# Kernel tuning notes

Hardware: AMD Instinct MI355X
Metric: run time of the kernel (lower is better)

## Reference

```python
import jax, jax.numpy as jnp
import numpy as np

WH, WW = 7, 7
N_HEADS = 6
INPUT_DIM = 192
HEAD_DIM = INPUT_DIM // N_HEADS
QK_SCALE = HEAD_DIM ** (-0.5)


def _relative_position_index(wh, ww):
    coords = np.stack(np.meshgrid(np.arange(wh), np.arange(ww), indexing='ij'))  # (2, wh, ww)
    cf = coords.reshape(2, -1)                       # (2, N)
    rel = cf[:, :, None] - cf[:, None, :]            # (2, N, N)
    rel = rel.transpose(1, 2, 0).copy()              # (N, N, 2)
    rel[:, :, 0] += wh - 1
    rel[:, :, 1] += ww - 1
    rel[:, :, 0] *= 2 * ww - 1
    return jnp.asarray(rel.sum(-1), dtype=jnp.int32)  # (N, N)

_REL_IDX = _relative_position_index(WH, WW)


def setup_inputs() -> dict:
    key = jax.random.key(0)
    ks = jax.random.split(key, 7)
    bW, nW = 4096, 64
    N = WH * WW
    s = 0.02
    return {
        "x": jax.random.normal(ks[0], (bW, WH, WW, INPUT_DIM), jnp.float32),
        "mask": jax.random.normal(ks[1], (nW, N, N), jnp.float32),
        "qkv_w": jax.random.normal(ks[2], (3 * INPUT_DIM, INPUT_DIM), jnp.float32) * s,
        "qkv_b": jax.random.normal(ks[3], (3 * INPUT_DIM,), jnp.float32) * s,
        "out_w": jax.random.normal(ks[4], (INPUT_DIM, INPUT_DIM), jnp.float32) * s,
        "out_b": jax.random.normal(ks[5], (INPUT_DIM,), jnp.float32) * s,
        "rpb_table": jax.random.normal(ks[6], ((2 * WH - 1) * (2 * WW - 1), N_HEADS), jnp.float32) * s,
    }


def reference(x, mask, qkv_w, qkv_b, out_w, out_b, rpb_table):
    b, Wh, Ww, C = x.shape
    N = Wh * Ww
    H, D = N_HEADS, HEAD_DIM
    # 1x1 conv == pointwise linear over channels-last input
    qkv = jnp.einsum('bxyc,oc->bxyo', x, qkv_w) + qkv_b          # (b, Wh, Ww, 3C)
    qkv = qkv.reshape(b, N, 3, H, D)                             # chunk order q,k,v; (h d) channel layout
    q, k, v = qkv[:, :, 0], qkv[:, :, 1], qkv[:, :, 2]           # (b, N, H, D)
    q = q * QK_SCALE
    sim = jnp.einsum('bihd,bjhd->bhij', q, k)                    # (b, H, N, N)
    # relative position bias gather
    rpb = rpb_table[_REL_IDX]                                    # (N, N, H)
    sim = sim + rpb.transpose(2, 0, 1)[None]                     # + (1, H, N, N)
    # shift mask add over windows
    nW = mask.shape[0]
    sim = sim.reshape(b // nW, nW, H, N, N) + mask[None, :, None]
    attn = jax.nn.softmax(sim, axis=-1).reshape(b, H, N, N)
    out = jnp.einsum('bhij,bjhd->bihd', attn, v)                 # (b, N, H, D)
    out = out.reshape(b, N, H * D)                               # (h d) channel order
    out = jnp.einsum('bnc,oc->bno', out, out_w) + out_b
    return out.reshape(b, Wh, Ww, C)
```

## Files before the change

kernel.cpp:

```cpp
#include <hip/hip_runtime.h>
#include <hip/hip_bf16.h>

typedef __bf16 bf16;
typedef __bf16 bf16x8 __attribute__((ext_vector_type(8)));
typedef float f32x4 __attribute__((ext_vector_type(4)));
typedef float floatv4 __attribute__((ext_vector_type(4)));

#define QK_SCALE 0.17677669529663687f

__device__ __forceinline__ bf16* qk_ptr(bf16* base, int row, int col) {
    return base + row * 32 + ((((col >> 3) ^ ((row >> 1) & 3)) << 3)) + (col & 7);
}
__device__ __forceinline__ bf16* vt_ptr(bf16* base, int row, int col) {
    return base + row * 64 + ((((col >> 3) ^ (row & 7)) << 3)) + (col & 7);
}
__device__ __forceinline__ bf16* ao_ptr(bf16* base, int row, int col) {
    return base + row * 192 + ((((col >> 3) ^ (row & 7)) << 3)) + (col & 7);
}

__global__ void wmsa_prep(const float* __restrict__ qkv_w,
                          const float* __restrict__ out_w,
                          const float* __restrict__ rpb_table,
                          const float* __restrict__ mask,
                          bf16* __restrict__ qkv_wb,
                          bf16* __restrict__ out_wb,
                          float* __restrict__ rpbx,
                          float* __restrict__ combo,
                          int build_combo) {
    int t = blockIdx.x * 256 + threadIdx.x;
    if (t < 110592) qkv_wb[t] = (bf16)qkv_w[t];
    if (t < 36864)  out_wb[t] = (bf16)out_w[t];
    if (t < 14406) {
        int h = t / 2401, ij = t % 2401, i = ij / 49, j = ij % 49;
        int ri = (i / 7 - j / 7 + 6) * 13 + (i % 7 - j % 7 + 6);
        rpbx[t] = rpb_table[ri * 6 + h];
    }
    if (build_combo && t < 64 * 6 * 64 * 64) {
        int j = t & 63, i = (t >> 6) & 63, r = t >> 12;
        int h = r % 6, w = r / 6;
        float v = -1e30f;
        if (i < 49 && j < 49) {
            int ri = (i / 7 - j / 7 + 6) * 13 + (i % 7 - j % 7 + 6);
            v = rpb_table[ri * 6 + h] + mask[w * 2401 + i * 49 + j];
        }
        combo[t] = v;
    }
}

template <bool USE_COMBO>
__global__ __launch_bounds__(768, 3) void wmsa_fused(
    const float* __restrict__ x, const float* __restrict__ mask,
    const float* __restrict__ qkv_b, const float* __restrict__ out_b,
    const bf16* __restrict__ qkv_wb, const bf16* __restrict__ out_wb,
    const float* __restrict__ rpbx, const float* __restrict__ combo,
    float* __restrict__ out)
{
    __shared__ __align__(16) bf16 s_x[12288];
    __shared__ __align__(16) bf16 s_qp[6][2048];
    __shared__ __align__(16) bf16 s_kao[12288];
    __shared__ __align__(16) bf16 s_vt[6][2048];

    const int b    = blockIdx.x;
    const int tid  = threadIdx.x;
    const int wv   = tid >> 6;
    const int lane = tid & 63;
    const int lo   = lane & 15;
    const int hi   = lane >> 4;

    const float* xw    = x + (size_t)b * 9408;
    const int    obase = wv * 48;
    const int    sec   = wv >> 2;

    {
        const int c0 = tid;
        const int r0s = c0 / 24, cc0 = c0 % 24;
        const float* p0 = xw + r0s * 192 + cc0 * 8;
        floatv4 f0 = *(const floatv4*)p0;
        floatv4 f1 = *(const floatv4*)(p0 + 4);
        bf16x8 v;
        v[0]=(bf16)f0[0]; v[1]=(bf16)f0[1]; v[2]=(bf16)f0[2]; v[3]=(bf16)f0[3];
        v[4]=(bf16)f1[0]; v[5]=(bf16)f1[1]; v[6]=(bf16)f1[2]; v[7]=(bf16)f1[3];
        *(bf16x8*)&s_x[(r0s * 24 + (cc0 ^ (r0s & 7))) * 8] = v;

        const int c1 = tid + 768;
        const int r1s = c1 / 24, cc1 = c1 % 24;
        bf16x8 w = {};
        if (r1s < 49) {
            const float* p1 = xw + r1s * 192 + cc1 * 8;
            floatv4 g0 = *(const floatv4*)p1;
            floatv4 g1 = *(const floatv4*)(p1 + 4);
            w[0]=(bf16)g0[0]; w[1]=(bf16)g0[1]; w[2]=(bf16)g0[2]; w[3]=(bf16)g0[3];
            w[4]=(bf16)g1[0]; w[5]=(bf16)g1[1]; w[6]=(bf16)g1[2]; w[7]=(bf16)g1[3];
        }
        *(bf16x8*)&s_x[(r1s * 24 + (cc1 ^ (r1s & 7))) * 8] = w;
    }
    __syncthreads();

#pragma unroll 1
    for (int mib = 0; mib < 2; ++mib) {
        f32x4 acc[2][3];
#pragma unroll
        for (int mi = 0; mi < 2; ++mi)
#pragma unroll
            for (int nj = 0; nj < 3; ++nj) acc[mi][nj] = (f32x4){0.f, 0.f, 0.f, 0.f};

        const int r0 = mib * 32 + lo;
        const int r1 = r0 + 16;

        auto loadB = [&](bf16x8* dst, int kk) {
#pragma unroll
            for (int nj = 0; nj < 3; ++nj)
                dst[nj] = *(const bf16x8*)(qkv_wb + (obase + nj * 16 + lo) * 192 + kk * 32 + hi * 8);
        };

        bf16x8 b0_[3], b1_[3], b2_[3];
        loadB(b0_, 0);
        loadB(b1_, 1);
#pragma unroll
        for (int kk = 0; kk < 6; ++kk) {
            if (kk < 4) loadB(b2_, kk + 2);
            bf16x8 a0 = *(const bf16x8*)ao_ptr(s_x, r0, kk * 32 + hi * 8);
            bf16x8 a1 = *(const bf16x8*)ao_ptr(s_x, r1, kk * 32 + hi * 8);
            acc[0][0] = __builtin_amdgcn_mfma_f32_16x16x32_bf16(a0, b0_[0], acc[0][0], 0, 0, 0);
            acc[1][0] = __builtin_amdgcn_mfma_f32_16x16x32_bf16(a1, b0_[0], acc[1][0], 0, 0, 0);
            acc[0][1] = __builtin_amdgcn_mfma_f32_16x16x32_bf16(a0, b0_[1], acc[0][1], 0, 0, 0);
            acc[1][1] = __builtin_amdgcn_mfma_f32_16x16x32_bf16(a1, b0_[1], acc[1][1], 0, 0, 0);
            acc[0][2] = __builtin_amdgcn_mfma_f32_16x16x32_bf16(a0, b0_[2], acc[0][2], 0, 0, 0);
            acc[1][2] = __builtin_amdgcn_mfma_f32_16x16x32_bf16(a1, b0_[2], acc[1][2], 0, 0, 0);
            b0_[0] = b1_[0]; b0_[1] = b1_[1]; b0_[2] = b1_[2];
            b1_[0] = b2_[0]; b1_[1] = b2_[1]; b1_[2] = b2_[2];
        }

#pragma unroll
        for (int nj = 0; nj < 3; ++nj) {
            const int o    = obase + nj * 16 + lo;
            const float bs = qkv_b[o];
            const int oc   = o - sec * 192;
            const int hh   = oc >> 5;
            const int dd   = oc & 31;
#pragma unroll
            for (int mi = 0; mi < 2; ++mi)
#pragma unroll
                for (int r = 0; r < 4; ++r) {
                    const int n = mib * 32 + mi * 16 + hi * 4 + r;
                    const float v = acc[mi][nj][r] + bs;
                    if (sec == 0)      *qk_ptr(&s_qp[hh][0], n, dd)      = (bf16)(v * QK_SCALE);
                    else if (sec == 1) *qk_ptr(s_kao + hh * 2048, n, dd) = (bf16)v;
                    else               *vt_ptr(&s_vt[hh][0], dd, n)      = (bf16)v;
                }
        }
    }
    __syncthreads();

    {
        const int h    = wv >> 1;
        const int p    = wv & 1;
        const int rowb = p * 32;
        bf16* qb    = &s_qp[h][0];
        bf16* kbase = s_kao + h * 2048;

        f32x4 cv[2][4];
        if (USE_COMBO) {
            const float* cb = combo + (((size_t)(b & 63) * 6 + h) << 12);
#pragma unroll
            for (int mi = 0; mi < 2; ++mi)
#pragma unroll
                for (int nt = 0; nt < 4; ++nt)
#pragma unroll
                    for (int r = 0; r < 4; ++r)
                        cv[mi][nt][r] = cb[(rowb + mi * 16 + hi * 4 + r) * 64 + nt * 16 + lo];
        }

        bf16x8 qa0 = *(const bf16x8*)qk_ptr(qb, rowb + lo, hi * 8);
        bf16x8 qa1 = *(const bf16x8*)qk_ptr(qb, rowb + 16 + lo, hi * 8);
        bf16x8 kb0 = *(const bf16x8*)qk_ptr(kbase,  0 + lo, hi * 8);
        bf16x8 kb1 = *(const bf16x8*)qk_ptr(kbase, 16 + lo, hi * 8);
        bf16x8 kb2 = *(const bf16x8*)qk_ptr(kbase, 32 + lo, hi * 8);
        bf16x8 kb3 = *(const bf16x8*)qk_ptr(kbase, 48 + lo, hi * 8);

        __syncthreads();

        f32x4 s[2][4];
#pragma unroll
        for (int mi = 0; mi < 2; ++mi)
#pragma unroll
            for (int nt = 0; nt < 4; ++nt) s[mi][nt] = (f32x4){0.f, 0.f, 0.f, 0.f};
        s[0][0] = __builtin_amdgcn_mfma_f32_16x16x32_bf16(qa0, kb0, s[0][0], 0, 0, 0);
        s[0][1] = __builtin_amdgcn_mfma_f32_16x16x32_bf16(qa0, kb1, s[0][1], 0, 0, 0);
        s[0][2] = __builtin_amdgcn_mfma_f32_16x16x32_bf16(qa0, kb2, s[0][2], 0, 0, 0);
        s[0][3] = __builtin_amdgcn_mfma_f32_16x16x32_bf16(qa0, kb3, s[0][3], 0, 0, 0);
        s[1][0] = __builtin_amdgcn_mfma_f32_16x16x32_bf16(qa1, kb0, s[1][0], 0, 0, 0);
        s[1][1] = __builtin_amdgcn_mfma_f32_16x16x32_bf16(qa1, kb1, s[1][1], 0, 0, 0);
        s[1][2] = __builtin_amdgcn_mfma_f32_16x16x32_bf16(qa1, kb2, s[1][2], 0, 0, 0);
        s[1][3] = __builtin_amdgcn_mfma_f32_16x16x32_bf16(qa1, kb3, s[1][3], 0, 0, 0);

        if (USE_COMBO) {
#pragma unroll
            for (int mi = 0; mi < 2; ++mi)
#pragma unroll
                for (int nt = 0; nt < 4; ++nt) s[mi][nt] += cv[mi][nt];
        } else {
            const float* mk = mask + (size_t)(b & 63) * 2401;
            const float* rb = rpbx + h * 2401;
#pragma unroll
            for (int nt = 0; nt < 4; ++nt) {
                const int j = nt * 16 + lo;
#pragma unroll
                for (int mi = 0; mi < 2; ++mi)
#pragma unroll
                    for (int r = 0; r < 4; ++r) {
                        const int i = rowb + mi * 16 + hi * 4 + r;
                        float sv = s[mi][nt][r];
                        if (j >= 49 || i >= 49) sv = -1e30f;
                        else sv += rb[i * 49 + j] + mk[i * 49 + j];
                        s[mi][nt][r] = sv;
                    }
            }
        }

#pragma unroll
        for (int mi = 0; mi < 2; ++mi)
#pragma unroll
            for (int r = 0; r < 4; ++r) {
                float m = fmaxf(fmaxf(s[mi][0][r], s[mi][1][r]),
                                fmaxf(s[mi][2][r], s[mi][3][r]));
                m = fmaxf(m, __shfl_xor(m, 1));
                m = fmaxf(m, __shfl_xor(m, 2));
                m = fmaxf(m, __shfl_xor(m, 4));
                m = fmaxf(m, __shfl_xor(m, 8));
                float sum = 0.f;
#pragma unroll
                for (int nt = 0; nt < 4; ++nt) {
                    float pv = __expf(s[mi][nt][r] - m);
                    s[mi][nt][r] = pv;
                    sum += pv;
                }
                sum += __shfl_xor(sum, 1);
                sum += __shfl_xor(sum, 2);
                sum += __shfl_xor(sum, 4);
                sum += __shfl_xor(sum, 8);
                const float inv = 1.0f / sum;
#pragma unroll
                for (int nt = 0; nt < 4; ++nt) s[mi][nt][r] *= inv;
            }

        f32x4 o00 = (f32x4){0.f,0.f,0.f,0.f}, o01 = (f32x4){0.f,0.f,0.f,0.f};
        f32x4 o10 = (f32x4){0.f,0.f,0.f,0.f}, o11 = (f32x4){0.f,0.f,0.f,0.f};
#pragma unroll
        for (int kk = 0; kk < 2; ++kk) {
#pragma unroll
            for (int mi = 0; mi < 2; ++mi)
#pragma unroll
                for (int c = 0; c < 2; ++c) {
                    const int nt = kk * 2 + c;
#pragma unroll
                    for (int r = 0; r < 4; ++r)
                        *qk_ptr(qb, rowb + mi * 16 + hi * 4 + r, c * 16 + lo) =
                            (bf16)s[mi][nt][r];
                }
            bf16x8 pa0 = *(const bf16x8*)qk_ptr(qb, rowb + lo, hi * 8);
            bf16x8 pa1 = *(const bf16x8*)qk_ptr(qb, rowb + 16 + lo, hi * 8);
            bf16x8 vb0 = *(const bf16x8*)vt_ptr(&s_vt[h][0],  0 + lo, kk * 32 + hi * 8);
            bf16x8 vb1 = *(const bf16x8*)vt_ptr(&s_vt[h][0], 16 + lo, kk * 32 + hi * 8);
            o00 = __builtin_amdgcn_mfma_f32_16x16x32_bf16(pa0, vb0, o00, 0, 0, 0);
            o10 = __builtin_amdgcn_mfma_f32_16x16x32_bf16(pa1, vb0, o10, 0, 0, 0);
            o01 = __builtin_amdgcn_mfma_f32_16x16x32_bf16(pa0, vb1, o01, 0, 0, 0);
            o11 = __builtin_amdgcn_mfma_f32_16x16x32_bf16(pa1, vb1, o11, 0, 0, 0);
        }

#pragma unroll
        for (int r = 0; r < 4; ++r) {
            const int n0 = rowb + hi * 4 + r;
            const int n1 = n0 + 16;
            *ao_ptr(s_kao, n0, h * 32 +  0 + lo) = (bf16)o00[r];
            *ao_ptr(s_kao, n0, h * 32 + 16 + lo) = (bf16)o01[r];
            *ao_ptr(s_kao, n1, h * 32 +  0 + lo) = (bf16)o10[r];
            *ao_ptr(s_kao, n1, h * 32 + 16 + lo) = (bf16)o11[r];
        }
    }
    __syncthreads();

    {
        const int o2 = wv * 16 + lo;
        f32x4 facc[4];
#pragma unroll
        for (int mi = 0; mi < 4; ++mi) facc[mi] = (f32x4){0.f, 0.f, 0.f, 0.f};

        bf16x8 fbc = *(const bf16x8*)(out_wb + o2 * 192 + hi * 8);
#pragma unroll
        for (int kk = 0; kk < 6; ++kk) {
            bf16x8 fbn;
            if (kk < 5) fbn = *(const bf16x8*)(out_wb + o2 * 192 + (kk + 1) * 32 + hi * 8);
            bf16x8 fa[4];
#pragma unroll
            for (int mi = 0; mi < 4; ++mi)
                fa[mi] = *(const bf16x8*)ao_ptr(s_kao, mi * 16 + lo, kk * 32 + hi * 8);
#pragma unroll
            for (int mi = 0; mi < 4; ++mi)
                facc[mi] = __builtin_amdgcn_mfma_f32_16x16x32_bf16(fa[mi], fbc, facc[mi], 0, 0, 0);
            fbc = fbn;
        }

        const float ob = out_b[o2];
        float* ow = out + (size_t)b * 9408;
#pragma unroll
        for (int mi = 0; mi < 4; ++mi)
#pragma unroll
            for (int r = 0; r < 4; ++r) {
                const int n = mi * 16 + hi * 4 + r;
                if (n < 49) ow[n * 192 + o2] = facc[mi][r] + ob;
            }
    }
}

extern "C" void kernel_launch(void* const* d_in, const int* in_sizes, int n_in,
                              void* d_out, int out_size, void* d_ws, size_t ws_size,
                              hipStream_t stream) {
    const float* x      = (const float*)d_in[0];
    const float* mask   = (const float*)d_in[1];
    const float* qkv_w  = (const float*)d_in[2];
    const float* qkv_b  = (const float*)d_in[3];
    const float* out_w  = (const float*)d_in[4];
    const float* out_b  = (const float*)d_in[5];
    const float* rpb    = (const float*)d_in[6];
    float* out          = (float*)d_out;

    char* ws = (char*)d_ws;
    bf16*  qkv_wb = (bf16*)ws;
    bf16*  out_wb = (bf16*)(ws + 221184);
    float* rpbx   = (float*)(ws + 294912);
    float* combo  = (float*)(ws + 352768);
    const bool use_combo = ws_size >= (size_t)(352768 + 6291456);

    hipLaunchKernelGGL(wmsa_prep, dim3(6144), dim3(256), 0, stream,
                       qkv_w, out_w, rpb, mask, qkv_wb, out_wb, rpbx, combo,
                       use_combo ? 1 : 0);
    if (use_combo)
        hipLaunchKernelGGL(HIP_KERNEL_NAME(wmsa_fused<true>), dim3(4096), dim3(768), 0, stream,
                           x, mask, qkv_b, out_b, qkv_wb, out_wb, rpbx, combo, out);
    else
        hipLaunchKernelGGL(HIP_KERNEL_NAME(wmsa_fused<false>), dim3(4096), dim3(768), 0, stream,
                           x, mask, qkv_b, out_b, qkv_wb, out_wb, rpbx, combo, out);
}
```

Baseline: 309.0 us.

## Make fused WMSA kernel persistent over 16 windows with double-buffered x prefetch

```diff
diff --git a/kernel.cpp b/kernel.cpp
--- a/kernel.cpp
+++ b/kernel.cpp
@@ -6,7 +6,8 @@
 typedef float f32x4 __attribute__((ext_vector_type(4)));
 typedef float floatv4 __attribute__((ext_vector_type(4)));
 
-#define QK_SCALE 0.17677669529663687f
+#define LOG2E 1.4426950408889634f
+#define QK_SCALE2 (0.17677669529663687f * 1.4426950408889634f)
 
 __device__ __forceinline__ bf16* qk_ptr(bf16* base, int row, int col) {
     return base + row * 32 + ((((col >> 3) ^ ((row >> 1) & 3)) << 3)) + (col & 7);
@@ -14,7 +15,7 @@
 __device__ __forceinline__ bf16* vt_ptr(bf16* base, int row, int col) {
     return base + row * 64 + ((((col >> 3) ^ (row & 7)) << 3)) + (col & 7);
 }
-__device__ __forceinline__ bf16* ao_ptr(bf16* base, int row, int col) {
+__device__ __forceinline__ bf16* t192_ptr(bf16* base, int row, int col) {
     return base + row * 192 + ((((col >> 3) ^ (row & 7)) << 3)) + (col & 7);
 }
 
@@ -41,11 +42,13 @@
         float v = -1e30f;
         if (i < 49 && j < 49) {
             int ri = (i / 7 - j / 7 + 6) * 13 + (i % 7 - j % 7 + 6);
-            v = rpb_table[ri * 6 + h] + mask[w * 2401 + i * 49 + j];
+            v = (rpb_table[ri * 6 + h] + mask[w * 2401 + i * 49 + j]) * LOG2E;
         }
         combo[t] = v;
     }
 }
+
+#define WIN_PER_BLK 16
 
 template <bool USE_COMBO>
 __global__ __launch_bounds__(768, 3) void wmsa_fused(
@@ -55,261 +58,295 @@
     const float* __restrict__ rpbx, const float* __restrict__ combo,
     float* __restrict__ out)
 {
-    __shared__ __align__(16) bf16 s_x[12288];
+    __shared__ __align__(16) bf16 s_x[2][12288];
     __shared__ __align__(16) bf16 s_qp[6][2048];
     __shared__ __align__(16) bf16 s_kao[12288];
     __shared__ __align__(16) bf16 s_vt[6][2048];
 
-    const int b    = blockIdx.x;
     const int tid  = threadIdx.x;
     const int wv   = tid >> 6;
     const int lane = tid & 63;
     const int lo   = lane & 15;
     const int hi   = lane >> 4;
 
-    const float* xw    = x + (size_t)b * 9408;
-    const int    obase = wv * 48;
-    const int    sec   = wv >> 2;
+    const int obase = wv * 48;
+    const int sec   = wv >> 2;
+    const int ah    = wv >> 1;
+    const int arow  = (wv & 1) * 32;
+
+    const int pr0 = tid / 24,         pcc0 = tid % 24;
+    const int pr1 = (tid + 768) / 24, pcc1 = (tid + 768) % 24;
+
+    const int bbase = blockIdx.x * WIN_PER_BLK;
 
     {
-        const int c0 = tid;
-        const int r0s = c0 / 24, cc0 = c0 % 24;
-        const float* p0 = xw + r0s * 192 + cc0 * 8;
+        const float* xw = x + (size_t)bbase * 9408;
+        const float* p0 = xw + pr0 * 192 + pcc0 * 8;
         floatv4 f0 = *(const floatv4*)p0;
         floatv4 f1 = *(const floatv4*)(p0 + 4);
         bf16x8 v;
         v[0]=(bf16)f0[0]; v[1]=(bf16)f0[1]; v[2]=(bf16)f0[2]; v[3]=(bf16)f0[3];
         v[4]=(bf16)f1[0]; v[5]=(bf16)f1[1]; v[6]=(bf16)f1[2]; v[7]=(bf16)f1[3];
-        *(bf16x8*)&s_x[(r0s * 24 + (cc0 ^ (r0s & 7))) * 8] = v;
-
-        const int c1 = tid + 768;
-        const int r1s = c1 / 24, cc1 = c1 % 24;
+        *(bf16x8*)&s_x[0][(pr0 * 24 + (pcc0 ^ (pr0 & 7))) * 8] = v;
+
         bf16x8 w = {};
-        if (r1s < 49) {
-            const float* p1 = xw + r1s * 192 + cc1 * 8;
+        if (pr1 < 49) {
+            const float* p1 = xw + pr1 * 192 + pcc1 * 8;
             floatv4 g0 = *(const floatv4*)p1;
             floatv4 g1 = *(const floatv4*)(p1 + 4);
             w[0]=(bf16)g0[0]; w[1]=(bf16)g0[1]; w[2]=(bf16)g0[2]; w[3]=(bf16)g0[3];
             w[4]=(bf16)g1[0]; w[5]=(bf16)g1[1]; w[6]=(bf16)g1[2]; w[7]=(bf16)g1[3];
         }
-        *(bf16x8*)&s_x[(r1s * 24 + (cc1 ^ (r1s & 7))) * 8] = w;
+        *(bf16x8*)&s_x[0][(pr1 * 24 + (pcc1 ^ (pr1 & 7))) * 8] = w;
     }
-    __syncthreads();
 
 #pragma unroll 1
-    for (int mib = 0; mib < 2; ++mib) {
-        f32x4 acc[2][3];
-#pragma unroll
-        for (int mi = 0; mi < 2; ++mi)
-#pragma unroll
-            for (int nj = 0; nj < 3; ++nj) acc[mi][nj] = (f32x4){0.f, 0.f, 0.f, 0.f};
-
-        const int r0 = mib * 32 + lo;
-        const int r1 = r0 + 16;
-
-        auto loadB = [&](bf16x8* dst, int kk) {
-#pragma unroll
-            for (int nj = 0; nj < 3; ++nj)
-                dst[nj] = *(const bf16x8*)(qkv_wb + (obase + nj * 16 + lo) * 192 + kk * 32 + hi * 8);
-        };
-
-        bf16x8 b0_[3], b1_[3], b2_[3];
-        loadB(b0_, 0);
-        loadB(b1_, 1);
-#pragma unroll
-        for (int kk = 0; kk < 6; ++kk) {
-            if (kk < 4) loadB(b2_, kk + 2);
-            bf16x8 a0 = *(const bf16x8*)ao_ptr(s_x, r0, kk * 32 + hi * 8);
-            bf16x8 a1 = *(const bf16x8*)ao_ptr(s_x, r1, kk * 32 + hi * 8);
-            acc[0][0] = __builtin_amdgcn_mfma_f32_16x16x32_bf16(a0, b0_[0], acc[0][0], 0, 0, 0);
-            acc[1][0] = __builtin_amdgcn_mfma_f32_16x16x32_bf16(a1, b0_[0], acc[1][0], 0, 0, 0);
-            acc[0][1] = __builtin_amdgcn_mfma_f32_16x16x32_bf16(a0, b0_[1], acc[0][1], 0, 0, 0);
-            acc[1][1] = __builtin_amdgcn_mfma_f32_16x16x32_bf16(a1, b0_[1], acc[1][1], 0, 0, 0);
-            acc[0][2] = __builtin_amdgcn_mfma_f32_16x16x32_bf16(a0, b0_[2], acc[0][2], 0, 0, 0);
-            acc[1][2] = __builtin_amdgcn_mfma_f32_16x16x32_bf16(a1, b0_[2], acc[1][2], 0, 0, 0);
-            b0_[0] = b1_[0]; b0_[1] = b1_[1]; b0_[2] = b1_[2];
-            b1_[0] = b2_[0]; b1_[1] = b2_[1]; b1_[2] = b2_[2];
-        }
-
-#pragma unroll
-        for (int nj = 0; nj < 3; ++nj) {
-            const int o    = obase + nj * 16 + lo;
-            const float bs = qkv_b[o];
-            const int oc   = o - sec * 192;
-            const int hh   = oc >> 5;
-            const int dd   = oc & 31;
+    for (int it = 0; it < WIN_PER_BLK; ++it) {
+        const int b = bbase + it;
+        bf16* sx = &s_x[it & 1][0];
+
+        __syncthreads();
+
+#pragma unroll 1
+        for (int mib = 0; mib < 2; ++mib) {
+            f32x4 acc[2][3];
 #pragma unroll
             for (int mi = 0; mi < 2; ++mi)
 #pragma unroll
+                for (int nj = 0; nj < 3; ++nj) acc[mi][nj] = (f32x4){0.f, 0.f, 0.f, 0.f};
+
+            const int r0 = mib * 32 + lo;
+            const int r1 = r0 + 16;
+
+            auto loadB = [&](bf16x8* dst, int kk) {
+#pragma unroll
+                for (int nj = 0; nj < 3; ++nj)
+                    dst[nj] = *(const bf16x8*)(qkv_wb + (obase + nj * 16 + lo) * 192 + kk * 32 + hi * 8);
+            };
+
+            bf16x8 b0_[3], b1_[3], b2_[3];
+            loadB(b0_, 0);
+            loadB(b1_, 1);
+#pragma unroll
+            for (int kk = 0; kk < 6; ++kk) {
+                if (kk < 4) loadB(b2_, kk + 2);
+                bf16x8 a0 = *(const bf16x8*)t192_ptr(sx, r0, kk * 32 + hi * 8);
+                bf16x8 a1 = *(const bf16x8*)t192_ptr(sx, r1, kk * 32 + hi * 8);
+                acc[0][0] = __builtin_amdgcn_mfma_f32_16x16x32_bf16(a0, b0_[0], acc[0][0], 0, 0, 0);
+                acc[1][0] = __builtin_amdgcn_mfma_f32_16x16x32_bf16(a1, b0_[0], acc[1][0], 0, 0, 0);
+                acc[0][1] = __builtin_amdgcn_mfma_f32_16x16x32_bf16(a0, b0_[1], acc[0][1], 0, 0, 0);
+                acc[1][1] = __builtin_amdgcn_mfma_f32_16x16x32_bf16(a1, b0_[1], acc[1][1], 0, 0, 0);
+                acc[0][2] = __builtin_amdgcn_mfma_f32_16x16x32_bf16(a0, b0_[2], acc[0][2], 0, 0, 0);
+                acc[1][2] = __builtin_amdgcn_mfma_f32_16x16x32_bf16(a1, b0_[2], acc[1][2], 0, 0, 0);
+                b0_[0] = b1_[0]; b0_[1] = b1_[1]; b0_[2] = b1_[2];
+                b1_[0] = b2_[0]; b1_[1] = b2_[1]; b1_[2] = b2_[2];
+            }
+
+#pragma unroll
+            for (int nj = 0; nj < 3; ++nj) {
+                const int o    = obase + nj * 16 + lo;
+                const float bs = qkv_b[o];
+                const int oc   = o - sec * 192;
+                const int hh   = oc >> 5;
+                const int dd   = oc & 31;
+#pragma unroll
+                for (int mi = 0; mi < 2; ++mi)
+#pragma unroll
+                    for (int r = 0; r < 4; ++r) {
+                        const int n = mib * 32 + mi * 16 + hi * 4 + r;
+                        const float v = acc[mi][nj][r] + bs;
+                        if (sec == 0)      *qk_ptr(&s_qp[hh][0], n, dd)      = (bf16)(v * QK_SCALE2);
+                        else if (sec == 1) *qk_ptr(s_kao + hh * 2048, n, dd) = (bf16)v;
+                        else               *vt_ptr(&s_vt[hh][0], dd, n)      = (bf16)v;
+                    }
+            }
+        }
+        __syncthreads();
+
+        {
+            bf16* qb    = &s_qp[ah][0];
+            bf16* kbase = s_kao + ah * 2048;
+
+            f32x4 cv[2][4];
+            if (USE_COMBO) {
+                const float* cb = combo + (((size_t)(b & 63) * 6 + ah) << 12);
+#pragma unroll
+                for (int mi = 0; mi < 2; ++mi)
+#pragma unroll
+                    for (int nt = 0; nt < 4; ++nt)
+#pragma unroll
+                        for (int r = 0; r < 4; ++r)
+                            cv[mi][nt][r] = cb[(arow + mi * 16 + hi * 4 + r) * 64 + nt * 16 + lo];
+            }
+
+            bf16x8 qa0 = *(const bf16x8*)qk_ptr(qb, arow + lo, hi * 8);
+            bf16x8 qa1 = *(const bf16x8*)qk_ptr(qb, arow + 16 + lo, hi * 8);
+            bf16x8 kb0 = *(const bf16x8*)qk_ptr(kbase,  0 + lo, hi * 8);
+            bf16x8 kb1 = *(const bf16x8*)qk_ptr(kbase, 16 + lo, hi * 8);
+            bf16x8 kb2 = *(const bf16x8*)qk_ptr(kbase, 32 + lo, hi * 8);
+            bf16x8 kb3 = *(const bf16x8*)qk_ptr(kbase, 48 + lo, hi * 8);
+
+            __syncthreads();
+
+            f32x4 s[2][4];
+#pragma unroll
+            for (int mi = 0; mi < 2; ++mi)
+#pragma unroll
+                for (int nt = 0; nt < 4; ++nt) s[mi][nt] = (f32x4){0.f, 0.f, 0.f, 0.f};
+            s[0][0] = __builtin_amdgcn_mfma_f32_16x16x32_bf16(qa0, kb0, s[0][0], 0, 0, 0);
+            s[0][1] = __builtin_amdgcn_mfma_f32_16x16x32_bf16(qa0, kb1, s[0][1], 0, 0, 0);
+            s[0][2] = __builtin_amdgcn_mfma_f32_16x16x32_bf16(qa0, kb2, s[0][2], 0, 0, 0);
+            s[0][3] = __builtin_amdgcn_mfma_f32_16x16x32_bf16(qa0, kb3, s[0][3], 0, 0, 0);
+            s[1][0] = __builtin_amdgcn_mfma_f32_16x16x32_bf16(qa1, kb0, s[1][0], 0, 0, 0);
+            s[1][1] = __builtin_amdgcn_mfma_f32_16x16x32_bf16(qa1, kb1, s[1][1], 0, 0, 0);
+            s[1][2] = __builtin_amdgcn_mfma_f32_16x16x32_bf16(qa1, kb2, s[1][2], 0, 0, 0);
+            s[1][3] = __builtin_amdgcn_mfma_f32_16x16x32_bf16(qa1, kb3, s[1][3], 0, 0, 0);
+
+            if (USE_COMBO) {
+#pragma unroll
+                for (int mi = 0; mi < 2; ++mi)
+#pragma unroll
+                    for (int nt = 0; nt < 4; ++nt) s[mi][nt] += cv[mi][nt];
+            } else {
+                const float* mk = mask + (size_t)(b & 63) * 2401;
+                const float* rb = rpbx + ah * 2401;
+#pragma unroll
+                for (int nt = 0; nt < 4; ++nt) {
+                    const int j = nt * 16 + lo;
+#pragma unroll
+                    for (int mi = 0; mi < 2; ++mi)
+#pragma unroll
+                        for (int r = 0; r < 4; ++r) {
+                            const int i = arow + mi * 16 + hi * 4 + r;
+                            float sv = s[mi][nt][r];
+                            if (j >= 49 || i >= 49) sv = -1e30f;
+                            else sv += (rb[i * 49 + j] + mk[i * 49 + j]) * LOG2E;
+                            s[mi][nt][r] = sv;
+                        }
+                }
+            }
+
+#pragma unroll
+            for (int mi = 0; mi < 2; ++mi)
+#pragma unroll
                 for (int r = 0; r < 4; ++r) {
-                    const int n = mib * 32 + mi * 16 + hi * 4 + r;
-                    const float v = acc[mi][nj][r] + bs;
-                    if (sec == 0)      *qk_ptr(&s_qp[hh][0], n, dd)      = (bf16)(v * QK_SCALE);
-                    else if (sec == 1) *qk_ptr(s_kao + hh * 2048, n, dd) = (bf16)v;
-                    else               *vt_ptr(&s_vt[hh][0], dd, n)      = (bf16)v;
+                    float m = fmaxf(fmaxf(s[mi][0][r], s[mi][1][r]),
+                                    fmaxf(s[mi][2][r], s[mi][3][r]));
+                    m = fmaxf(m, __shfl_xor(m, 1));
+                    m = fmaxf(m, __shfl_xor(m, 2));
+                    m = fmaxf(m, __shfl_xor(m, 4));
+                    m = fmaxf(m, __shfl_xor(m, 8));
+                    float sum = 0.f;
+#pragma unroll
+                    for (int nt = 0; nt < 4; ++nt) {
+                        float pv = exp2f(s[mi][nt][r] - m);
+                        s[mi][nt][r] = pv;
+                        sum += pv;
+                    }
+                    sum += __shfl_xor(sum, 1);
+                    sum += __shfl_xor(sum, 2);
+                    sum += __shfl_xor(sum, 4);
+                    sum += __shfl_xor(sum, 8);
+                    const float inv = 1.0f / sum;
+#pragma unroll
+                    for (int nt = 0; nt < 4; ++nt) s[mi][nt][r] *= inv;
                 }
-        }
-    }
-    __syncthreads();
-
-    {
-        const int h    = wv >> 1;
-        const int p    = wv & 1;
-        const int rowb = p * 32;
-        bf16* qb    = &s_qp[h][0];
-        bf16* kbase = s_kao + h * 2048;
-
-        f32x4 cv[2][4];
-        if (USE_COMBO) {
-            const float* cb = combo + (((size_t)(b & 63) * 6 + h) << 12);
-#pragma unroll
-            for (int mi = 0; mi < 2; ++mi)
-#pragma unroll
-                for (int nt = 0; nt < 4; ++nt)
-#pragma unroll
-                    for (int r = 0; r < 4; ++r)
-                        cv[mi][nt][r] = cb[(rowb + mi * 16 + hi * 4 + r) * 64 + nt * 16 + lo];
-        }
-
-        bf16x8 qa0 = *(const bf16x8*)qk_ptr(qb, rowb + lo, hi * 8);
-        bf16x8 qa1 = *(const bf16x8*)qk_ptr(qb, rowb + 16 + lo, hi * 8);
-        bf16x8 kb0 = *(const bf16x8*)qk_ptr(kbase,  0 + lo, hi * 8);
-        bf16x8 kb1 = *(const bf16x8*)qk_ptr(kbase, 16 + lo, hi * 8);
-        bf16x8 kb2 = *(const bf16x8*)qk_ptr(kbase, 32 + lo, hi * 8);
-        bf16x8 kb3 = *(const bf16x8*)qk_ptr(kbase, 48 + lo, hi * 8);
-
+
+            f32x4 o00 = (f32x4){0.f,0.f,0.f,0.f}, o01 = (f32x4){0.f,0.f,0.f,0.f};
+            f32x4 o10 = (f32x4){0.f,0.f,0.f,0.f}, o11 = (f32x4){0.f,0.f,0.f,0.f};
+#pragma unroll
+            for (int kk = 0; kk < 2; ++kk) {
+#pragma unroll
+                for (int mi = 0; mi < 2; ++mi)
+#pragma unroll
+                    for (int c = 0; c < 2; ++c) {
+                        const int nt = kk * 2 + c;
+#pragma unroll
+                        for (int r = 0; r < 4; ++r)
+                            *qk_ptr(qb, arow + mi * 16 + hi * 4 + r, c * 16 + lo) =
+                                (bf16)s[mi][nt][r];
+                    }
+                bf16x8 pa0 = *(const bf16x8*)qk_ptr(qb, arow + lo, hi * 8);
+                bf16x8 pa1 = *(const bf16x8*)qk_ptr(qb, arow + 16 + lo, hi * 8);
+                bf16x8 vb0 = *(const bf16x8*)vt_ptr(&s_vt[ah][0],  0 + lo, kk * 32 + hi * 8);
+                bf16x8 vb1 = *(const bf16x8*)vt_ptr(&s_vt[ah][0], 16 + lo, kk * 32 + hi * 8);
+                o00 = __builtin_amdgcn_mfma_f32_16x16x32_bf16(pa0, vb0, o00, 0, 0, 0);
+                o10 = __builtin_amdgcn_mfma_f32_16x16x32_bf16(pa1, vb0, o10, 0, 0, 0);
+                o01 = __builtin_amdgcn_mfma_f32_16x16x32_bf16(pa0, vb1, o01, 0, 0, 0);
+                o11 = __builtin_amdgcn_mfma_f32_16x16x32_bf16(pa1, vb1, o11, 0, 0, 0);
+            }
+
+#pragma unroll
+            for (int r = 0; r < 4; ++r) {
+                const int n0 = arow + hi * 4 + r;
+                const int n1 = n0 + 16;
+                *t192_ptr(s_kao, n0, ah * 32 +  0 + lo) = (bf16)o00[r];
+                *t192_ptr(s_kao, n0, ah * 32 + 16 + lo) = (bf16)o01[r];
+                *t192_ptr(s_kao, n1, ah * 32 +  0 + lo) = (bf16)o10[r];
+                *t192_ptr(s_kao, n1, ah * 32 + 16 + lo) = (bf16)o11[r];
+            }
+        }
         __syncthreads();
 
-        f32x4 s[2][4];
-#pragma unroll
-        for (int mi = 0; mi < 2; ++mi)
-#pragma unroll
-            for (int nt = 0; nt < 4; ++nt) s[mi][nt] = (f32x4){0.f, 0.f, 0.f, 0.f};
-        s[0][0] = __builtin_amdgcn_mfma_f32_16x16x32_bf16(qa0, kb0, s[0][0], 0, 0, 0);
-        s[0][1] = __builtin_amdgcn_mfma_f32_16x16x32_bf16(qa0, kb1, s[0][1], 0, 0, 0);
-        s[0][2] = __builtin_amdgcn_mfma_f32_16x16x32_bf16(qa0, kb2, s[0][2], 0, 0, 0);
-        s[0][3] = __builtin_amdgcn_mfma_f32_16x16x32_bf16(qa0, kb3, s[0][3], 0, 0, 0);
-        s[1][0] = __builtin_amdgcn_mfma_f32_16x16x32_bf16(qa1, kb0, s[1][0], 0, 0, 0);
-        s[1][1] = __builtin_amdgcn_mfma_f32_16x16x32_bf16(qa1, kb1, s[1][1], 0, 0, 0);
-        s[1][2] = __builtin_amdgcn_mfma_f32_16x16x32_bf16(qa1, kb2, s[1][2], 0, 0, 0);
-        s[1][3] = __builtin_amdgcn_mfma_f32_16x16x32_bf16(qa1, kb3, s[1][3], 0, 0, 0);
-
-        if (USE_COMBO) {
-#pragma unroll
-            for (int mi = 0; mi < 2; ++mi)
-#pragma unroll
-                for (int nt = 0; nt < 4; ++nt) s[mi][nt] += cv[mi][nt];
-        } else {
-            const float* mk = mask + (size_t)(b & 63) * 2401;
-            const float* rb = rpbx + h * 2401;
-#pragma unroll
-            for (int nt = 0; nt < 4; ++nt) {
-                const int j = nt * 16 + lo;
-#pragma unroll
-                for (int mi = 0; mi < 2; ++mi)
-#pragma unroll
-                    for (int r = 0; r < 4; ++r) {
-                        const int i = rowb + mi * 16 + hi * 4 + r;
-                        float sv = s[mi][nt][r];
-                        if (j >= 49 || i >= 49) sv = -1e30f;
-                        else sv += rb[i * 49 + j] + mk[i * 49 + j];
-                        s[mi][nt][r] = sv;
-                    }
-            }
-        }
-
-#pragma unroll
-        for (int mi = 0; mi < 2; ++mi)
-#pragma unroll
-            for (int r = 0; r < 4; ++r) {
-                float m = fmaxf(fmaxf(s[mi][0][r], s[mi][1][r]),
-                                fmaxf(s[mi][2][r], s[mi][3][r]));
-                m = fmaxf(m, __shfl_xor(m, 1));
-                m = fmaxf(m, __shfl_xor(m, 2));
-                m = fmaxf(m, __shfl_xor(m, 4));
-                m = fmaxf(m, __shfl_xor(m, 8));
-                float sum = 0.f;
-#pragma unroll
-                for (int nt = 0; nt < 4; ++nt) {
-                    float pv = __expf(s[mi][nt][r] - m);
-                    s[mi][nt][r] = pv;
-                    sum += pv;
+        floatv4 pf00, pf01, pf10, pf11;
+        const bool do_pf = (it + 1 < WIN_PER_BLK);
+        if (do_pf) {
+            const float* xn = x + (size_t)(b + 1) * 9408;
+            const float* p0 = xn + pr0 * 192 + pcc0 * 8;
+            pf00 = *(const floatv4*)p0;
+            pf01 = *(const floatv4*)(p0 + 4);
+            pf10 = (floatv4){0.f,0.f,0.f,0.f};
+            pf11 = (floatv4){0.f,0.f,0.f,0.f};
+            if (pr1 < 49) {
+                const float* p1 = xn + pr1 * 192 + pcc1 * 8;
+                pf10 = *(const floatv4*)p1;
+                pf11 = *(const floatv4*)(p1 + 4);
+            }
+        }
+
+        {
+            const int o2 = wv * 16 + lo;
+            f32x4 facc[4];
+#pragma unroll
+            for (int mi = 0; mi < 4; ++mi) facc[mi] = (f32x4){0.f, 0.f, 0.f, 0.f};
+
+            bf16x8 fbc = *(const bf16x8*)(out_wb + o2 * 192 + hi * 8);
+#pragma unroll
+            for (int kk = 0; kk < 6; ++kk) {
+                bf16x8 fbn;
+                if (kk < 5) fbn = *(const bf16x8*)(out_wb + o2 * 192 + (kk + 1) * 32 + hi * 8);
+                bf16x8 fa[4];
+#pragma unroll
+                for (int mi = 0; mi < 4; ++mi)
+                    fa[mi] = *(const bf16x8*)t192_ptr(s_kao, mi * 16 + lo, kk * 32 + hi * 8);
+#pragma unroll
+                for (int mi = 0; mi < 4; ++mi)
+                    facc[mi] = __builtin_amdgcn_mfma_f32_16x16x32_bf16(fa[mi], fbc, facc[mi], 0, 0, 0);
+                fbc = fbn;
+            }
+
+            const float ob = out_b[o2];
+            float* ow = out + (size_t)b * 9408;
+#pragma unroll
+            for (int mi = 0; mi < 4; ++mi)
+#pragma unroll
+                for (int r = 0; r < 4; ++r) {
+                    const int n = mi * 16 + hi * 4 + r;
+                    if (n < 49) ow[n * 192 + o2] = facc[mi][r] + ob;
                 }
-                sum += __shfl_xor(sum, 1);
-                sum += __shfl_xor(sum, 2);
-                sum += __shfl_xor(sum, 4);
-                sum += __shfl_xor(sum, 8);
-                const float inv = 1.0f / sum;
-#pragma unroll
-                for (int nt = 0; nt < 4; ++nt) s[mi][nt][r] *= inv;
-            }
-
-        f32x4 o00 = (f32x4){0.f,0.f,0.f,0.f}, o01 = (f32x4){0.f,0.f,0.f,0.f};
-        f32x4 o10 = (f32x4){0.f,0.f,0.f,0.f}, o11 = (f32x4){0.f,0.f,0.f,0.f};
-#pragma unroll
-        for (int kk = 0; kk < 2; ++kk) {
-#pragma unroll
-            for (int mi = 0; mi < 2; ++mi)
-#pragma unroll
-                for (int c = 0; c < 2; ++c) {
-                    const int nt = kk * 2 + c;
-#pragma unroll
-                    for (int r = 0; r < 4; ++r)
-                        *qk_ptr(qb, rowb + mi * 16 + hi * 4 + r, c * 16 + lo) =
-                            (bf16)s[mi][nt][r];
-                }
-            bf16x8 pa0 = *(const bf16x8*)qk_ptr(qb, rowb + lo, hi * 8);
-            bf16x8 pa1 = *(const bf16x8*)qk_ptr(qb, rowb + 16 + lo, hi * 8);
-            bf16x8 vb0 = *(const bf16x8*)vt_ptr(&s_vt[h][0],  0 + lo, kk * 32 + hi * 8);
-            bf16x8 vb1 = *(const bf16x8*)vt_ptr(&s_vt[h][0], 16 + lo, kk * 32 + hi * 8);
-            o00 = __builtin_amdgcn_mfma_f32_16x16x32_bf16(pa0, vb0, o00, 0, 0, 0);
-            o10 = __builtin_amdgcn_mfma_f32_16x16x32_bf16(pa1, vb0, o10, 0, 0, 0);
-            o01 = __builtin_amdgcn_mfma_f32_16x16x32_bf16(pa0, vb1, o01, 0, 0, 0);
-            o11 = __builtin_amdgcn_mfma_f32_16x16x32_bf16(pa1, vb1, o11, 0, 0, 0);
-        }
-
-#pragma unroll
-        for (int r = 0; r < 4; ++r) {
-            const int n0 = rowb + hi * 4 + r;
-            const int n1 = n0 + 16;
-            *ao_ptr(s_kao, n0, h * 32 +  0 + lo) = (bf16)o00[r];
-            *ao_ptr(s_kao, n0, h * 32 + 16 + lo) = (bf16)o01[r];
-            *ao_ptr(s_kao, n1, h * 32 +  0 + lo) = (bf16)o10[r];
-            *ao_ptr(s_kao, n1, h * 32 + 16 + lo) = (bf16)o11[r];
-        }
-    }
-    __syncthreads();
-
-    {
-        const int o2 = wv * 16 + lo;
-        f32x4 facc[4];
-#pragma unroll
-        for (int mi = 0; mi < 4; ++mi) facc[mi] = (f32x4){0.f, 0.f, 0.f, 0.f};
-
-        bf16x8 fbc = *(const bf16x8*)(out_wb + o2 * 192 + hi * 8);
-#pragma unroll
-        for (int kk = 0; kk < 6; ++kk) {
-            bf16x8 fbn;
-            if (kk < 5) fbn = *(const bf16x8*)(out_wb + o2 * 192 + (kk + 1) * 32 + hi * 8);
-            bf16x8 fa[4];
-#pragma unroll
-            for (int mi = 0; mi < 4; ++mi)
-                fa[mi] = *(const bf16x8*)ao_ptr(s_kao, mi * 16 + lo, kk * 32 + hi * 8);
-#pragma unroll
-            for (int mi = 0; mi < 4; ++mi)
-                facc[mi] = __builtin_amdgcn_mfma_f32_16x16x32_bf16(fa[mi], fbc, facc[mi], 0, 0, 0);
-            fbc = fbn;
-        }
-
-        const float ob = out_b[o2];
-        float* ow = out + (size_t)b * 9408;
-#pragma unroll
-        for (int mi = 0; mi < 4; ++mi)
-#pragma unroll
-            for (int r = 0; r < 4; ++r) {
-                const int n = mi * 16 + hi * 4 + r;
-                if (n < 49) ow[n * 192 + o2] = facc[mi][r] + ob;
-            }
+        }
+
+        if (do_pf) {
+            bf16* xb = &s_x[(it + 1) & 1][0];
+            bf16x8 v;
+            v[0]=(bf16)pf00[0]; v[1]=(bf16)pf00[1]; v[2]=(bf16)pf00[2]; v[3]=(bf16)pf00[3];
+            v[4]=(bf16)pf01[0]; v[5]=(bf16)pf01[1]; v[6]=(bf16)pf01[2]; v[7]=(bf16)pf01[3];
+            *(bf16x8*)&xb[(pr0 * 24 + (pcc0 ^ (pr0 & 7))) * 8] = v;
+            bf16x8 w;
+            w[0]=(bf16)pf10[0]; w[1]=(bf16)pf10[1]; w[2]=(bf16)pf10[2]; w[3]=(bf16)pf10[3];
+            w[4]=(bf16)pf11[0]; w[5]=(bf16)pf11[1]; w[6]=(bf16)pf11[2]; w[7]=(bf16)pf11[3];
+            *(bf16x8*)&xb[(pr1 * 24 + (pcc1 ^ (pr1 & 7))) * 8] = w;
+        }
     }
 }
 
@@ -336,9 +373,9 @@
                        qkv_w, out_w, rpb, mask, qkv_wb, out_wb, rpbx, combo,
                        use_combo ? 1 : 0);
     if (use_combo)
-        hipLaunchKernelGGL(HIP_KERNEL_NAME(wmsa_fused<true>), dim3(4096), dim3(768), 0, stream,
+        hipLaunchKernelGGL(HIP_KERNEL_NAME(wmsa_fused<true>), dim3(256), dim3(768), 0, stream,
                            x, mask, qkv_b, out_b, qkv_wb, out_wb, rpbx, combo, out);
     else
-        hipLaunchKernelGGL(HIP_KERNEL_NAME(wmsa_fused<false>), dim3(4096), dim3(768), 0, stream,
+        hipLaunchKernelGGL(HIP_KERNEL_NAME(wmsa_fused<false>), dim3(256), dim3(768), 0, stream,
                            x, mask, qkv_b, out_b, qkv_wb, out_wb, rpbx, combo, out);
 }
```

Measured after the change: 540.2 us. 1.75x slower.
